# Kernel tuning notes

Hardware: AMD Instinct MI355X
Metric: run time of the kernel (lower is better)

The kernel has to match this reference:

```python
import jax, jax.numpy as jnp
import numpy as np

EMBED = 1024
HEADS = 16
DEPTH = EMBED // HEADS
FFN_DIM = 4096
EPS = 1e-9


def layer_norm(x, g, b):
    mu = jnp.mean(x, axis=-1, keepdims=True)
    var = jnp.mean(jnp.square(x - mu), axis=-1, keepdims=True)
    return (x - mu) * jax.lax.rsqrt(var + EPS) * g + b


def setup_inputs() -> dict:
    key = jax.random.key(0)
    ks = jax.random.split(key, 16)
    B, S = 2, 2048
    s_e = 1.0 / np.sqrt(EMBED)
    s_f = 1.0 / np.sqrt(FFN_DIM)
    return {
        "x": jax.random.normal(ks[0], (B, S, EMBED), dtype=jnp.float32),
        "mask": jnp.zeros((B, 1, 1, S), dtype=jnp.float32),
        "wq_w": jax.random.normal(ks[1], (EMBED, EMBED), dtype=jnp.float32) * s_e,
        "wq_b": jnp.zeros((EMBED,), dtype=jnp.float32),
        "wk_w": jax.random.normal(ks[2], (EMBED, EMBED), dtype=jnp.float32) * s_e,
        "wk_b": jnp.zeros((EMBED,), dtype=jnp.float32),
        "wv_w": jax.random.normal(ks[3], (EMBED, EMBED), dtype=jnp.float32) * s_e,
        "wv_b": jnp.zeros((EMBED,), dtype=jnp.float32),
        "wo_w": jax.random.normal(ks[4], (EMBED, EMBED), dtype=jnp.float32) * s_e,
        "wo_b": jnp.zeros((EMBED,), dtype=jnp.float32),
        "f1_w": jax.random.normal(ks[5], (EMBED, FFN_DIM), dtype=jnp.float32) * s_e,
        "f1_b": jnp.zeros((FFN_DIM,), dtype=jnp.float32),
        "f2_w": jax.random.normal(ks[6], (FFN_DIM, EMBED), dtype=jnp.float32) * s_f,
        "f2_b": jnp.zeros((EMBED,), dtype=jnp.float32),
        "ln1_g": jnp.ones((EMBED,), dtype=jnp.float32),
        "ln1_b": jnp.zeros((EMBED,), dtype=jnp.float32),
        "ln2_g": jnp.ones((EMBED,), dtype=jnp.float32),
        "ln2_b": jnp.zeros((EMBED,), dtype=jnp.float32),
    }


def reference(x, mask, wq_w, wq_b, wk_w, wk_b, wv_w, wv_b, wo_w, wo_b,
              f1_w, f1_b, f2_w, f2_b, ln1_g, ln1_b, ln2_g, ln2_b):
    B, S, E = x.shape

    def split_heads(t):  # (B,S,E) -> (B,H,S,D)
        return t.reshape(B, S, HEADS, DEPTH).transpose(0, 2, 1, 3)

    q = split_heads(x @ wq_w + wq_b)
    k = split_heads(x @ wk_w + wk_b)
    v = split_heads(x @ wv_w + wv_b)

    logits = jnp.einsum("bhqd,bhkd->bhqk", q, k) / jnp.sqrt(jnp.float32(DEPTH))
    logits = logits + mask * -1e12  # mask broadcast (B,1,1,S)
    attn = jax.nn.softmax(logits, axis=-1)
    out = jnp.einsum("bhqk,bhkd->bhqd", attn, v)
    out = out.transpose(0, 2, 1, 3).reshape(B, S, E)
    out = out @ wo_w + wo_b

    # dropout is identity (is_train=False)
    h = layer_norm(out + x, ln1_g, ln1_b)
    f = jax.nn.relu(h @ f1_w + f1_b) @ f2_w + f2_b
    return layer_norm(f + h, ln2_g, ln2_b)
```

## Files before the change

kernel.cpp:

```cpp
#include <hip/hip_runtime.h>
#include <hip/hip_bf16.h>
#include <stdint.h>

typedef __hip_bfloat16 bf16;
typedef __attribute__((ext_vector_type(8))) short short8;
typedef __attribute__((ext_vector_type(4))) short short4v;
typedef __attribute__((ext_vector_type(4))) float floatx4;

#define E_DIM 1024
#define S_LEN 2048
#define NB    2
#define NH    16
#define HD    64
#define FFN   4096
#define MTOT  4096

__device__ __forceinline__ void gl_lds16(const void* g, void* l) {
  __builtin_amdgcn_global_load_lds(
      (__attribute__((address_space(1))) void*)(g),
      (__attribute__((address_space(3))) void*)(l), 16, 0, 0);
}

__device__ __forceinline__ int fswz_v(int row) { return row & 7; }
__device__ __forceinline__ int fswz_k(int row) {
  return ((row ^ (row >> 3)) & 3) | ((((row >> 3) ^ (row >> 4)) & 1) << 2);
}

__device__ __forceinline__ float bf16bits2float(short s) {
  union { unsigned u; float f; } c;
  c.u = ((unsigned)(unsigned short)s) << 16;
  return c.f;
}

__global__ __launch_bounds__(256)
void cvt_bf16(const float* __restrict__ in, bf16* __restrict__ out) {
  const size_t i = ((size_t)blockIdx.x * 256 + threadIdx.x) * 4;
  float4 v = *(const float4*)(in + i);
  out[i + 0] = __float2bfloat16(v.x);
  out[i + 1] = __float2bfloat16(v.y);
  out[i + 2] = __float2bfloat16(v.z);
  out[i + 3] = __float2bfloat16(v.w);
}

__global__ __launch_bounds__(256)
void transpose_all(const float* __restrict__ wq, const float* __restrict__ wk,
                   const float* __restrict__ wv, const float* __restrict__ wo,
                   const float* __restrict__ f1, const float* __restrict__ f2,
                   bf16* __restrict__ W3T, bf16* __restrict__ woT,
                   bf16* __restrict__ f1T, bf16* __restrict__ f2T) {
  const int z = blockIdx.z;
  const float* in;
  bf16* out;
  int inStride, outStride, rOff, cOff;
  if (z < 4) {
    in = (z == 0) ? wq : (z == 1) ? wk : (z == 2) ? wv : wo;
    out = (z < 3) ? (W3T + (size_t)z * 1024 * 1024) : woT;
    inStride = 1024; outStride = 1024; rOff = 0; cOff = 0;
  } else if (z < 8) {
    in = f1; out = f1T; inStride = 4096; outStride = 1024;
    rOff = 0; cOff = (z - 4) * 1024;
  } else {
    in = f2; out = f2T; inStride = 1024; outStride = 4096;
    rOff = (z - 8) * 1024; cOff = 0;
  }
  __shared__ float tile[32][33];
  const int tx = threadIdx.x & 31;
  const int ty = threadIdx.x >> 5;
  const int c0 = blockIdx.x * 32;
  const int r0 = blockIdx.y * 32;
#pragma unroll
  for (int j = 0; j < 32; j += 8)
    tile[ty + j][tx] =
        in[(size_t)(rOff + r0 + ty + j) * inStride + cOff + c0 + tx];
  __syncthreads();
#pragma unroll
  for (int j = 0; j < 32; j += 8)
    out[(size_t)(cOff + c0 + ty + j) * outStride + rOff + r0 + tx] =
        __float2bfloat16(tile[tx][ty + j]);
}

__global__ __launch_bounds__(256)
void prep_bias(const float* __restrict__ qb, const float* __restrict__ kb,
               const float* __restrict__ vb, float* __restrict__ out) {
  const int i = blockIdx.x * 256 + threadIdx.x;
  float v = (i < 1024) ? qb[i] * 0.125f
                       : ((i < 2048) ? kb[i - 1024] : vb[i - 2048]);
  out[i] = v;
}

__global__ __launch_bounds__(256)
void gemm_bt(const bf16* __restrict__ A, const bf16* __restrict__ B,
             const float* __restrict__ bias, void* __restrict__ Cout,
             int M, int N, int Kpart, int lda, int mode) {
  __shared__ alignas(16) bf16 sA[128 * 32];
  __shared__ alignas(16) bf16 sB[128 * 32];
  const int tid   = threadIdx.x;
  const int wave  = tid >> 6;
  const int lane  = tid & 63;
  const int row16 = lane & 15;
  const int quad  = lane >> 4;
  const int m0 = blockIdx.x * 128;
  const int n0 = blockIdx.y * 128;
  const int wm = (wave >> 1) * 64;
  const int wn = (wave & 1) * 64;
  const int koff = blockIdx.z * Kpart;

  floatx4 acc[4][4];
#pragma unroll
  for (int i = 0; i < 4; i++)
#pragma unroll
    for (int j = 0; j < 4; j++) {
      floatx4 z = {0.f, 0.f, 0.f, 0.f};
      acc[i][j] = z;
    }

  for (int k0 = koff; k0 < koff + Kpart; k0 += 32) {
#pragma unroll
    for (int j = 0; j < 2; ++j) {
      const int chunk = wave * 2 + j;
      const int e = chunk * 512 + lane * 8;
      const int r = e >> 5;
      const int kk = e & 31;
      gl_lds16(A + (size_t)(m0 + r) * lda + k0 + kk, sA + chunk * 512);
      gl_lds16(B + (size_t)(n0 + r) * lda + k0 + kk, sB + chunk * 512);
    }
    __syncthreads();

    short8 af[4], bfr[4];
#pragma unroll
    for (int i = 0; i < 4; i++) {
      af[i]  = *(const short8*)(sA + (wm + i * 16 + row16) * 32 + quad * 8);
      bfr[i] = *(const short8*)(sB + (wn + i * 16 + row16) * 32 + quad * 8);
    }
#pragma unroll
    for (int mi = 0; mi < 4; mi++)
#pragma unroll
      for (int ni = 0; ni < 4; ni++)
        acc[mi][ni] = __builtin_amdgcn_mfma_f32_16x16x32_bf16(
            af[mi], bfr[ni], acc[mi][ni], 0, 0, 0);
    __syncthreads();
  }

  float bval[4] = {0.f, 0.f, 0.f, 0.f};
  if (mode != 0) {
#pragma unroll
    for (int ni = 0; ni < 4; ni++) bval[ni] = bias[n0 + wn + ni * 16 + row16];
  }

#pragma unroll
  for (int mi = 0; mi < 4; mi++) {
#pragma unroll
    for (int ni = 0; ni < 4; ni++) {
      const int col = n0 + wn + ni * 16 + row16;
      if (mode == 0) {
        float* co = (float*)Cout + (size_t)blockIdx.z * M * N;
#pragma unroll
        for (int r = 0; r < 4; r++) {
          const int row = m0 + wm + mi * 16 + quad * 4 + r;
          co[(size_t)row * N + col] = acc[mi][ni][r];
        }
      } else if (mode == 1) {
#pragma unroll
        for (int r = 0; r < 4; r++) {
          const int row = m0 + wm + mi * 16 + quad * 4 + r;
          float v = acc[mi][ni][r] + bval[ni];
          v = v > 0.f ? v : 0.f;
          ((bf16*)Cout)[(size_t)row * N + col] = __float2bfloat16(v);
        }
      } else {
        const int mat = col >> 10;
        const int c10 = col & 1023;
        const int hh = c10 >> 6, dd = c10 & 63;
        const float scl = (mat == 0) ? 0.125f : 1.0f;
        bf16* qout = (bf16*)Cout;
        const int rbase = m0 + wm + mi * 16 + quad * 4;
        const int b = rbase >> 11, s = rbase & 2047;
        const size_t bh = (size_t)b * NH + hh;
        if (mat == 2) {
          bf16* vt = qout + (1 << 23);
          short4v pv;
#pragma unroll
          for (int r = 0; r < 4; r++) {
            bf16 t = __float2bfloat16(acc[mi][ni][r] + bval[ni]);
            pv[r] = *(short*)&t;
          }
          *(short4v*)(vt + (bh * HD + dd) * S_LEN + s) = pv;
        } else {
          bf16* o = (mat == 1) ? (qout + (1 << 22)) : qout;
#pragma unroll
          for (int r = 0; r < 4; r++) {
            float v = acc[mi][ni][r] * scl + bval[ni];
            o[(bh * S_LEN + s + r) * HD + dd] = __float2bfloat16(v);
          }
        }
      }
    }
  }
}

__global__ __launch_bounds__(256, 4)
void flash_attn(const bf16* __restrict__ Q, const bf16* __restrict__ K,
                const bf16* __restrict__ Vt, const float* __restrict__ mask,
                bf16* __restrict__ Out) {
  __shared__ alignas(16) bf16 sK[64 * 64];
  __shared__ alignas(16) bf16 sV[64 * 64];
  __shared__ alignas(16) float sM[S_LEN];

  const int tid   = threadIdx.x;
  const int wave  = tid >> 6;
  const int lane  = tid & 63;
  const int row16 = lane & 15;
  const int quad  = lane >> 4;
  const int bh = blockIdx.y;
  const int b = bh >> 4, h = bh & 15;
  const int q0 = blockIdx.x * 64;
  const int qg = q0 + wave * 16 + row16;

  const bf16* qp = Q + ((size_t)bh * S_LEN + qg) * HD;
  short8 qf0 = *(const short8*)(qp + quad * 8);
  short8 qf1 = *(const short8*)(qp + 32 + quad * 8);

  for (int i = tid; i < S_LEN / 4; i += 256) {
    float4 mv = ((const float4*)(mask + (size_t)b * S_LEN))[i];
    float4 w = {-1e12f * mv.x, -1e12f * mv.y, -1e12f * mv.z, -1e12f * mv.w};
    ((float4*)sM)[i] = w;
  }

  float m_i = -1e30f, l_i = 0.f;
  floatx4 ov[4];
#pragma unroll
  for (int i = 0; i < 4; i++) { floatx4 z = {0.f,0.f,0.f,0.f}; ov[i] = z; }

  const bf16* Kbase = K + (size_t)bh * S_LEN * HD;
  const bf16* Vbase = Vt + (size_t)bh * HD * S_LEN;

  for (int kt = 0; kt < S_LEN / 64; ++kt) {
    const bf16* Kg = Kbase + (size_t)kt * 64 * HD;
    const bf16* Vg = Vbase + kt * 64;
#pragma unroll
    for (int j = 0; j < 2; ++j) {
      const int ch = wave * 2 + j;
      const int row = ch * 8 + (lane >> 3);
      const int sc_ = lane & 7;
      gl_lds16(Kg + row * 64 + ((sc_ ^ fswz_k(row)) * 8), sK + ch * 512);
      gl_lds16(Vg + (size_t)row * S_LEN + ((sc_ ^ fswz_v(row)) * 8), sV + ch * 512);
    }
    __syncthreads();

    floatx4 sc[4];
#pragma unroll
    for (int mi = 0; mi < 4; mi++) {
      const int row = ((row16 >> 2) << 3) + (row16 & 3) + ((mi & 1) << 2) + ((mi >> 1) << 5);
      const int fk = fswz_k(row);
      short8 kf0 = *(const short8*)(sK + row * 64 + ((quad ^ fk) << 3));
      short8 kf1 = *(const short8*)(sK + row * 64 + (((4 + quad) ^ fk) << 3));
      floatx4 z = {0.f, 0.f, 0.f, 0.f};
      z = __builtin_amdgcn_mfma_f32_16x16x32_bf16(kf0, qf0, z, 0, 0, 0);
      sc[mi] = __builtin_amdgcn_mfma_f32_16x16x32_bf16(kf1, qf1, z, 0, 0, 0);
    }

#pragma unroll
    for (int mi = 0; mi < 4; mi++) {
      float4 mv = *(const float4*)(sM + kt * 64 + (quad << 3) + ((mi & 1) << 2) + ((mi >> 1) << 5));
      sc[mi][0] += mv.x; sc[mi][1] += mv.y; sc[mi][2] += mv.z; sc[mi][3] += mv.w;
    }

    float t = sc[0][0];
#pragma unroll
    for (int mi = 0; mi < 4; mi++)
#pragma unroll
      for (int r = 0; r < 4; r++) t = fmaxf(t, sc[mi][r]);
    t = fmaxf(t, __shfl_xor(t, 16));
    t = fmaxf(t, __shfl_xor(t, 32));
    const float m_new = fmaxf(m_i, t);
    const float alpha = __expf(m_i - m_new);
    m_i = m_new;
    float tsum = 0.f;
#pragma unroll
    for (int mi = 0; mi < 4; mi++)
#pragma unroll
      for (int r = 0; r < 4; r++) {
        float p = __expf(sc[mi][r] - m_new);
        sc[mi][r] = p;
        tsum += p;
      }
    tsum += __shfl_xor(tsum, 16);
    tsum += __shfl_xor(tsum, 32);
    l_i = l_i * alpha + tsum;

    short8 pf[2];
#pragma unroll
    for (int ks = 0; ks < 2; ks++)
#pragma unroll
      for (int jp = 0; jp < 4; jp++) {
        const int mi = 2 * ks + (jp >> 1);
        const int r0 = (jp & 1) * 2;
        bf16 p0 = __float2bfloat16(sc[mi][r0]);
        bf16 p1 = __float2bfloat16(sc[mi][r0 + 1]);
        pf[ks][2 * jp]     = *(short*)&p0;
        pf[ks][2 * jp + 1] = *(short*)&p1;
      }

#pragma unroll
    for (int mi = 0; mi < 4; mi++)
#pragma unroll
      for (int r = 0; r < 4; r++) ov[mi][r] *= alpha;
#pragma unroll
    for (int mi = 0; mi < 4; mi++) {
      const int row = mi * 16 + row16;
      const int fv = fswz_v(row);
      short8 v0 = *(const short8*)(sV + row * 64 + ((quad ^ fv) << 3));
      short8 v1 = *(const short8*)(sV + row * 64 + (((4 + quad) ^ fv) << 3));
      ov[mi] = __builtin_amdgcn_mfma_f32_16x16x32_bf16(v0, pf[0], ov[mi], 0, 0, 0);
      ov[mi] = __builtin_amdgcn_mfma_f32_16x16x32_bf16(v1, pf[1], ov[mi], 0, 0, 0);
    }
    __syncthreads();
  }

  const float inv = 1.0f / l_i;
#pragma unroll
  for (int mi = 0; mi < 4; mi++) {
    short4v pv;
#pragma unroll
    for (int r = 0; r < 4; r++) {
      bf16 t = __float2bfloat16(ov[mi][r] * inv);
      pv[r] = *(short*)&t;
    }
    *(short4v*)(Out + ((size_t)(b * S_LEN + qg)) * E_DIM + h * HD + mi * 16 + quad * 4) = pv;
  }
}

__global__ __launch_bounds__(256)
void ln_reduce(const float* __restrict__ p0, const float* __restrict__ p1,
               const float* __restrict__ resf, const bf16* __restrict__ resb,
               const float* __restrict__ bias, const float* __restrict__ g,
               const float* __restrict__ be, float* __restrict__ outf,
               bf16* __restrict__ outb) {
  const int row = blockIdx.x;
  const int tid = threadIdx.x;
  const size_t base = (size_t)row * 1024;
  const int c = tid * 4;
  float4 a = *(const float4*)(p0 + base + c);
  float4 bq = *(const float4*)(p1 + base + c);
  float4 rv;
  if (resf) {
    rv = *(const float4*)(resf + base + c);
  } else {
    short4v rb = *(const short4v*)((const short*)resb + base + c);
    rv.x = bf16bits2float(rb[0]);
    rv.y = bf16bits2float(rb[1]);
    rv.z = bf16bits2float(rb[2]);
    rv.w = bf16bits2float(rb[3]);
  }
  float4 bi = *(const float4*)(bias + c);
  float4 xv;
  xv.x = a.x + bq.x + rv.x + bi.x;
  xv.y = a.y + bq.y + rv.y + bi.y;
  xv.z = a.z + bq.z + rv.z + bi.z;
  xv.w = a.w + bq.w + rv.w + bi.w;
  float s  = xv.x + xv.y + xv.z + xv.w;
  float s2 = xv.x * xv.x + xv.y * xv.y + xv.z * xv.z + xv.w * xv.w;
#pragma unroll
  for (int d = 1; d < 64; d <<= 1) {
    s  += __shfl_xor(s, d);
    s2 += __shfl_xor(s2, d);
  }
  __shared__ float red[2][4];
  const int wave = tid >> 6;
  if ((tid & 63) == 0) { red[0][wave] = s; red[1][wave] = s2; }
  __syncthreads();
  s  = red[0][0] + red[0][1] + red[0][2] + red[0][3];
  s2 = red[1][0] + red[1][1] + red[1][2] + red[1][3];
  const float mu  = s * (1.0f / 1024.0f);
  const float var = s2 * (1.0f / 1024.0f) - mu * mu;
  const float rs  = rsqrtf(var + 1e-9f);
  float4 gg = *(const float4*)(g + c);
  float4 bb = *(const float4*)(be + c);
  float4 y;
  y.x = (xv.x - mu) * rs * gg.x + bb.x;
  y.y = (xv.y - mu) * rs * gg.y + bb.y;
  y.z = (xv.z - mu) * rs * gg.z + bb.z;
  y.w = (xv.w - mu) * rs * gg.w + bb.w;
  if (outf) *(float4*)(outf + base + c) = y;
  if (outb) {
    bf16* o = outb + base + c;
    o[0] = __float2bfloat16(y.x);
    o[1] = __float2bfloat16(y.y);
    o[2] = __float2bfloat16(y.z);
    o[3] = __float2bfloat16(y.w);
  }
}

extern "C" void kernel_launch(void* const* d_in, const int* in_sizes, int n_in,
                              void* d_out, int out_size, void* d_ws,
                              size_t ws_size, hipStream_t stream) {
  const float* x    = (const float*)d_in[0];
  const float* mask = (const float*)d_in[1];
  const float* wq_w = (const float*)d_in[2];
  const float* wq_b = (const float*)d_in[3];
  const float* wk_w = (const float*)d_in[4];
  const float* wk_b = (const float*)d_in[5];
  const float* wv_w = (const float*)d_in[6];
  const float* wv_b = (const float*)d_in[7];
  const float* wo_w = (const float*)d_in[8];
  const float* wo_b = (const float*)d_in[9];
  const float* f1_w = (const float*)d_in[10];
  const float* f1_b = (const float*)d_in[11];
  const float* f2_w = (const float*)d_in[12];
  const float* f2_b = (const float*)d_in[13];
  const float* ln1_g = (const float*)d_in[14];
  const float* ln1_b = (const float*)d_in[15];
  const float* ln2_g = (const float*)d_in[16];
  const float* ln2_b = (const float*)d_in[17];
  float* out = (float*)d_out;

  char* ws = (char*)d_ws;
  const size_t MB = 1u << 20;
  bf16*  xbf   = (bf16*)(ws + 0 * MB);
  bf16*  W3T   = (bf16*)(ws + 8 * MB);
  bf16*  woT   = (bf16*)(ws + 14 * MB);
  float* bqkv  = (float*)(ws + 16 * MB);
  bf16*  Qb    = (bf16*)(ws + 17 * MB);
  bf16*  attnb = (bf16*)(ws + 0 * MB);
  bf16*  ffn1  = (bf16*)(ws + 17 * MB);
  bf16*  f1T   = (bf16*)(ws + 49 * MB);
  bf16*  f2T   = (bf16*)(ws + 57 * MB);
  float* parts = (float*)(ws + 65 * MB);
  bf16*  hbf   = (bf16*)(ws + 97 * MB);
  const size_t PSTRIDE = (size_t)MTOT * E_DIM;

  cvt_bf16<<<4096, 256, 0, stream>>>(x, xbf);
  transpose_all<<<dim3(32, 32, 12), 256, 0, stream>>>(
      wq_w, wk_w, wv_w, wo_w, f1_w, f2_w, W3T, woT, f1T, f2T);
  prep_bias<<<12, 256, 0, stream>>>(wq_b, wk_b, wv_b, bqkv);

  gemm_bt<<<dim3(32, 24, 1), 256, 0, stream>>>(xbf, W3T, bqkv, Qb,
                                               MTOT, 3 * E_DIM, E_DIM, E_DIM, 2);

  flash_attn<<<dim3(S_LEN / 64, NB * NH), 256, 0, stream>>>(
      Qb, Qb + (1 << 22), Qb + (1 << 23), mask, attnb);

  gemm_bt<<<dim3(32, 8, 2), 256, 0, stream>>>(attnb, woT, nullptr, parts,
                                              MTOT, E_DIM, E_DIM / 2, E_DIM, 0);

  ln_reduce<<<MTOT, 256, 0, stream>>>(parts, parts + PSTRIDE, x, nullptr,
                                      wo_b, ln1_g, ln1_b, nullptr, hbf);

  gemm_bt<<<dim3(32, 32, 1), 256, 0, stream>>>(hbf, f1T, f1_b, ffn1,
                                               MTOT, FFN, E_DIM, E_DIM, 1);

  gemm_bt<<<dim3(32, 8, 2), 256, 0, stream>>>(ffn1, f2T, nullptr, parts,
                                              MTOT, E_DIM, FFN / 2, FFN, 0);

  ln_reduce<<<MTOT, 256, 0, stream>>>(parts, parts + PSTRIDE, nullptr, hbf,
                                      f2_b, ln2_g, ln2_b, out, nullptr);
}
```

Before: 399.1 us.

## Replace GEMM with 256x256 double-buffered tile kernel, XCD remap and 4-way split-K

The 128x128 single-buffered GEMM becomes a 512-thread kernel with 256x256 tiles and double-buffered LDS, so the global-to-LDS load of the next K slice overlaps the MFMA work on the current one. Block IDs are remapped to group work per XCD, and MFMA sections get raised wave priority. The output-projection and FFN2 GEMMs use 4-way split-K when the workspace is large enough, and the layernorm reduce sums four partials. The larger tiles cut the block count (e.g. 64 blocks per split for the N=1024 GEMMs), and the extra partials add memory traffic.

```diff
diff --git a/kernel.cpp b/kernel.cpp
--- a/kernel.cpp
+++ b/kernel.cpp
@@ -88,57 +88,92 @@
   out[i] = v;
 }
 
-__global__ __launch_bounds__(256)
-void gemm_bt(const bf16* __restrict__ A, const bf16* __restrict__ B,
+__global__ __launch_bounds__(512)
+void gemm256(const bf16* __restrict__ A, const bf16* __restrict__ B,
              const float* __restrict__ bias, void* __restrict__ Cout,
+             void* __restrict__ Cout2,
              int M, int N, int Kpart, int lda, int mode) {
-  __shared__ alignas(16) bf16 sA[128 * 32];
-  __shared__ alignas(16) bf16 sB[128 * 32];
+  __shared__ alignas(16) bf16 sA[2][256 * 32];
+  __shared__ alignas(16) bf16 sB[2][256 * 32];
   const int tid   = threadIdx.x;
   const int wave  = tid >> 6;
   const int lane  = tid & 63;
   const int row16 = lane & 15;
   const int quad  = lane >> 4;
-  const int m0 = blockIdx.x * 128;
-  const int n0 = blockIdx.y * 128;
-  const int wm = (wave >> 1) * 64;
-  const int wn = (wave & 1) * 64;
+
+  const int gx = gridDim.x;
+  const int nwg = gx * gridDim.y;
+  const int cpx = nwg >> 3;
+  int id = blockIdx.y * gx + blockIdx.x;
+  id = (id & 7) * cpx + (id >> 3);
+  const int m0 = (id % gx) * 256;
+  const int n0 = (id / gx) * 256;
+
+  const int wm = (wave >> 2) * 128;
+  const int wn = (wave & 3) * 64;
   const int koff = blockIdx.z * Kpart;
-
-  floatx4 acc[4][4];
-#pragma unroll
-  for (int i = 0; i < 4; i++)
+  const int NT = Kpart >> 5;
+
+  floatx4 acc[8][4];
+#pragma unroll
+  for (int i = 0; i < 8; i++)
 #pragma unroll
     for (int j = 0; j < 4; j++) {
       floatx4 z = {0.f, 0.f, 0.f, 0.f};
       acc[i][j] = z;
     }
 
-  for (int k0 = koff; k0 < koff + Kpart; k0 += 32) {
+  auto stage = [&](int t, int p) {
+    const int k0 = koff + t * 32;
 #pragma unroll
     for (int j = 0; j < 2; ++j) {
-      const int chunk = wave * 2 + j;
-      const int e = chunk * 512 + lane * 8;
-      const int r = e >> 5;
-      const int kk = e & 31;
-      gl_lds16(A + (size_t)(m0 + r) * lda + k0 + kk, sA + chunk * 512);
-      gl_lds16(B + (size_t)(n0 + r) * lda + k0 + kk, sB + chunk * 512);
-    }
-    __syncthreads();
-
-    short8 af[4], bfr[4];
-#pragma unroll
-    for (int i = 0; i < 4; i++) {
-      af[i]  = *(const short8*)(sA + (wm + i * 16 + row16) * 32 + quad * 8);
-      bfr[i] = *(const short8*)(sB + (wn + i * 16 + row16) * 32 + quad * 8);
-    }
-#pragma unroll
-    for (int mi = 0; mi < 4; mi++)
+      const int seg = wave * 2 + j;
+      const int r = seg * 16 + (lane >> 2);
+      const int c = (lane & 3) * 8;
+      gl_lds16(A + (size_t)(m0 + r) * lda + k0 + c, &sA[p][seg * 512]);
+      gl_lds16(B + (size_t)(n0 + r) * lda + k0 + c, &sB[p][seg * 512]);
+    }
+  };
+
+  auto compute = [&](int p) {
+    const bf16* sAp = sA[p];
+    const bf16* sBp = sB[p];
+    short8 bfr[4];
+#pragma unroll
+    for (int ni = 0; ni < 4; ni++)
+      bfr[ni] = *(const short8*)(sBp + (wn + ni * 16 + row16) * 32 + quad * 8);
+    __builtin_amdgcn_s_setprio(1);
+#pragma unroll
+    for (int mi = 0; mi < 8; mi++) {
+      short8 af = *(const short8*)(sAp + (wm + mi * 16 + row16) * 32 + quad * 8);
 #pragma unroll
       for (int ni = 0; ni < 4; ni++)
         acc[mi][ni] = __builtin_amdgcn_mfma_f32_16x16x32_bf16(
-            af[mi], bfr[ni], acc[mi][ni], 0, 0, 0);
-    __syncthreads();
+            af, bfr[ni], acc[mi][ni], 0, 0, 0);
+    }
+    __builtin_amdgcn_s_setprio(0);
+  };
+
+  stage(0, 0);
+  stage(1, 1);
+  asm volatile("s_waitcnt vmcnt(4)" ::: "memory");
+  __builtin_amdgcn_sched_barrier(0);
+  asm volatile("s_barrier" ::: "memory");
+
+  for (int t = 0; t < NT; ++t) {
+    const int p = t & 1;
+    compute(p);
+    asm volatile("s_waitcnt lgkmcnt(0)" ::: "memory");
+    __builtin_amdgcn_sched_barrier(0);
+    asm volatile("s_barrier" ::: "memory");
+    if (t + 2 < NT) {
+      stage(t + 2, p);
+      asm volatile("s_waitcnt vmcnt(4)" ::: "memory");
+    } else {
+      asm volatile("s_waitcnt vmcnt(0)" ::: "memory");
+    }
+    __builtin_amdgcn_sched_barrier(0);
+    asm volatile("s_barrier" ::: "memory");
   }
 
   float bval[4] = {0.f, 0.f, 0.f, 0.f};
@@ -148,12 +183,13 @@
   }
 
 #pragma unroll
-  for (int mi = 0; mi < 4; mi++) {
+  for (int mi = 0; mi < 8; mi++) {
 #pragma unroll
     for (int ni = 0; ni < 4; ni++) {
       const int col = n0 + wn + ni * 16 + row16;
       if (mode == 0) {
-        float* co = (float*)Cout + (size_t)blockIdx.z * M * N;
+        float* co = (float*)((blockIdx.z < 2) ? Cout : Cout2) +
+                    (size_t)(blockIdx.z & 1) * M * N;
 #pragma unroll
         for (int r = 0; r < 4; r++) {
           const int row = m0 + wm + mi * 16 + quad * 4 + r;
@@ -332,6 +368,7 @@
 
 __global__ __launch_bounds__(256)
 void ln_reduce(const float* __restrict__ p0, const float* __restrict__ p1,
+               const float* __restrict__ p2, const float* __restrict__ p3,
                const float* __restrict__ resf, const bf16* __restrict__ resb,
                const float* __restrict__ bias, const float* __restrict__ g,
                const float* __restrict__ be, float* __restrict__ outf,
@@ -342,6 +379,19 @@
   const int c = tid * 4;
   float4 a = *(const float4*)(p0 + base + c);
   float4 bq = *(const float4*)(p1 + base + c);
+  float4 xv;
+  xv.x = a.x + bq.x;
+  xv.y = a.y + bq.y;
+  xv.z = a.z + bq.z;
+  xv.w = a.w + bq.w;
+  if (p2) {
+    float4 a2 = *(const float4*)(p2 + base + c);
+    float4 a3 = *(const float4*)(p3 + base + c);
+    xv.x += a2.x + a3.x;
+    xv.y += a2.y + a3.y;
+    xv.z += a2.z + a3.z;
+    xv.w += a2.w + a3.w;
+  }
   float4 rv;
   if (resf) {
     rv = *(const float4*)(resf + base + c);
@@ -353,11 +403,10 @@
     rv.w = bf16bits2float(rb[3]);
   }
   float4 bi = *(const float4*)(bias + c);
-  float4 xv;
-  xv.x = a.x + bq.x + rv.x + bi.x;
-  xv.y = a.y + bq.y + rv.y + bi.y;
-  xv.z = a.z + bq.z + rv.z + bi.z;
-  xv.w = a.w + bq.w + rv.w + bi.w;
+  xv.x += rv.x + bi.x;
+  xv.y += rv.y + bi.y;
+  xv.z += rv.z + bi.z;
+  xv.w += rv.w + bi.w;
   float s  = xv.x + xv.y + xv.z + xv.w;
   float s2 = xv.x * xv.x + xv.y * xv.y + xv.z * xv.z + xv.w * xv.w;
 #pragma unroll
@@ -425,33 +474,38 @@
   bf16*  ffn1  = (bf16*)(ws + 17 * MB);
   bf16*  f1T   = (bf16*)(ws + 49 * MB);
   bf16*  f2T   = (bf16*)(ws + 57 * MB);
-  float* parts = (float*)(ws + 65 * MB);
+  float* P01   = (float*)(ws + 65 * MB);
   bf16*  hbf   = (bf16*)(ws + 97 * MB);
-  const size_t PSTRIDE = (size_t)MTOT * E_DIM;
+  float* P23   = (float*)(ws + 105 * MB);
+  const size_t PS = (size_t)MTOT * E_DIM;
+
+  const int KS = (ws_size >= (size_t)137 * MB) ? 4 : 2;
+  const float* p2 = (KS == 4) ? P23 : nullptr;
+  const float* p3 = (KS == 4) ? P23 + PS : nullptr;
 
   cvt_bf16<<<4096, 256, 0, stream>>>(x, xbf);
   transpose_all<<<dim3(32, 32, 12), 256, 0, stream>>>(
       wq_w, wk_w, wv_w, wo_w, f1_w, f2_w, W3T, woT, f1T, f2T);
   prep_bias<<<12, 256, 0, stream>>>(wq_b, wk_b, wv_b, bqkv);
 
-  gemm_bt<<<dim3(32, 24, 1), 256, 0, stream>>>(xbf, W3T, bqkv, Qb,
-                                               MTOT, 3 * E_DIM, E_DIM, E_DIM, 2);
+  gemm256<<<dim3(16, 12, 1), 512, 0, stream>>>(
+      xbf, W3T, bqkv, Qb, nullptr, MTOT, 3 * E_DIM, E_DIM, E_DIM, 2);
 
   flash_attn<<<dim3(S_LEN / 64, NB * NH), 256, 0, stream>>>(
       Qb, Qb + (1 << 22), Qb + (1 << 23), mask, attnb);
 
-  gemm_bt<<<dim3(32, 8, 2), 256, 0, stream>>>(attnb, woT, nullptr, parts,
-                                              MTOT, E_DIM, E_DIM / 2, E_DIM, 0);
-
-  ln_reduce<<<MTOT, 256, 0, stream>>>(parts, parts + PSTRIDE, x, nullptr,
+  gemm256<<<dim3(16, 4, KS), 512, 0, stream>>>(
+      attnb, woT, nullptr, P01, P23, MTOT, E_DIM, E_DIM / KS, E_DIM, 0);
+
+  ln_reduce<<<MTOT, 256, 0, stream>>>(P01, P01 + PS, p2, p3, x, nullptr,
                                       wo_b, ln1_g, ln1_b, nullptr, hbf);
 
-  gemm_bt<<<dim3(32, 32, 1), 256, 0, stream>>>(hbf, f1T, f1_b, ffn1,
-                                               MTOT, FFN, E_DIM, E_DIM, 1);
-
-  gemm_bt<<<dim3(32, 8, 2), 256, 0, stream>>>(ffn1, f2T, nullptr, parts,
-                                              MTOT, E_DIM, FFN / 2, FFN, 0);
-
-  ln_reduce<<<MTOT, 256, 0, stream>>>(parts, parts + PSTRIDE, nullptr, hbf,
+  gemm256<<<dim3(16, 16, 1), 512, 0, stream>>>(
+      hbf, f1T, f1_b, ffn1, nullptr, MTOT, FFN, E_DIM, E_DIM, 1);
+
+  gemm256<<<dim3(16, 4, KS), 512, 0, stream>>>(
+      ffn1, f2T, nullptr, P01, P23, MTOT, E_DIM, FFN / KS, FFN, 0);
+
+  ln_reduce<<<MTOT, 256, 0, stream>>>(P01, P01 + PS, p2, p3, nullptr, hbf,
                                       f2_b, ln2_g, ln2_b, out, nullptr);
 }
```

Measured after the change: 409.3 us. 1.03x slower.
